# Kernel optimization log

Hardware: AMD Instinct MI355X
Metric: run time of the kernel (lower is better)

## Reference

```python
import jax, jax.numpy as jnp
import numpy as np

NUM_HEADS = 16
NUM_KV_HEADS = 4
HEAD_DIM = 128
HALF_DIM = HEAD_DIM // 2
LAMBDA_INIT = 0.8
LAMBDA_MIN = 0.0
LAMBDA_MAX = 1.0
CAUSAL = True
NORMALIZE_DIFF = True
NEG = -1.0e9


def setup_inputs() -> dict:
    key = jax.random.key(0)
    k1, k2, k3 = jax.random.split(key, 3)
    B, Sq, Sk = 1, 2048, 2048
    query = jax.random.normal(k1, (B, NUM_HEADS, Sq, HEAD_DIM), dtype=jnp.float32)
    key_t = jax.random.normal(k2, (B, NUM_KV_HEADS, Sk, HEAD_DIM), dtype=jnp.float32)
    value = jax.random.normal(k3, (B, NUM_KV_HEADS, Sk, HEAD_DIM), dtype=jnp.float32)
    return {"query": query, "key": key_t, "value": value}


def reference(query, key, value):
    scale = 1.0 / (HALF_DIM ** 0.5)
    lam = jnp.clip(jnp.float32(LAMBDA_INIT), LAMBDA_MIN, LAMBDA_MAX)
    # GQA: repeat KV heads to match query heads
    rep = NUM_HEADS // NUM_KV_HEADS
    k = jnp.repeat(key, rep, axis=1)    # [b,h,k,d]
    v = jnp.repeat(value, rep, axis=1)  # [b,h,k,d]
    q1, q2 = query[..., :HALF_DIM], query[..., HALF_DIM:]
    k1, k2 = k[..., :HALF_DIM], k[..., HALF_DIM:]
    scores1 = jnp.einsum('bhqd,bhkd->bhqk', q1, k1) * scale
    scores2 = jnp.einsum('bhqd,bhkd->bhqk', q2, k2) * scale
    if CAUSAL:
        Sq, Sk = query.shape[2], k.shape[2]
        mask = jnp.tril(jnp.ones((Sq, Sk), dtype=jnp.float32))  # lower-triangular causal
        scores1 = scores1 * mask + (1.0 - mask) * NEG
        scores2 = scores2 * mask + (1.0 - mask) * NEG
    attn1 = jax.nn.softmax(scores1, axis=-1)
    attn2 = jax.nn.softmax(scores2, axis=-1)
    diff_attn = attn1 - lam * attn2
    out = jnp.einsum('bhqk,bhkd->bhqd', diff_attn, v)
    if NORMALIZE_DIFF:
        out = out * (1.0 - LAMBDA_INIT)
    return out
```

## Files before the change

kernel.cpp:

```cpp
#include <hip/hip_runtime.h>

#define NUM_HEADS 16
#define HEAD_DIM  128
#define SEQ       2048

typedef __attribute__((ext_vector_type(8))) unsigned short us8;
typedef __attribute__((ext_vector_type(8))) __bf16 bf16x8;
typedef __attribute__((ext_vector_type(4))) float f32x4;
typedef __attribute__((ext_vector_type(4))) unsigned u32x4;
typedef __attribute__((ext_vector_type(2))) unsigned u32x2;

static __device__ inline unsigned short f2bf(float x) {
    union { float f; unsigned u; } v; v.f = x;
    unsigned r = v.u + 0x7FFFu + ((v.u >> 16) & 1u);
    return (unsigned short)(r >> 16);
}
static __device__ inline float bf2f(unsigned short h) {
    union { float f; unsigned u; } v; v.u = ((unsigned)h) << 16;
    return v.f;
}
static __device__ inline unsigned pk2bf(float a, float b) {
    return (unsigned)f2bf(a) | ((unsigned)f2bf(b) << 16);
}
static __device__ inline float fast_exp2(float x) {
#if __has_builtin(__builtin_amdgcn_exp2f)
    return __builtin_amdgcn_exp2f(x);
#else
    return exp2f(x);
#endif
}
static __device__ inline f32x4 mfma16(us8 a, us8 b, f32x4 c) {
    return __builtin_amdgcn_mfma_f32_16x16x32_bf16(
        __builtin_bit_cast(bf16x8, a), __builtin_bit_cast(bf16x8, b), c, 0, 0, 0);
}

__global__ __launch_bounds__(256)
void prep_kv(const float* __restrict__ K, const float* __restrict__ V,
             unsigned short* __restrict__ Kbf, unsigned short* __restrict__ Vtb)
{
    const int bx = (int)blockIdx.x, t = (int)threadIdx.x;
    __shared__ __align__(16) float Ls[64][130];
    if (bx < 512) {
        const size_t base = ((size_t)bx * 256 + t) * 8;
        float x[8];
        *(float4*)&x[0] = *(const float4*)(K + base);
        *(float4*)&x[4] = *(const float4*)(K + base + 4);
        u32x4 pk;
        #pragma unroll
        for (int j = 0; j < 4; ++j) pk[j] = pk2bf(x[2*j], x[2*j+1]);
        *(us8*)(Kbf + base) = __builtin_bit_cast(us8, pk);
    } else {
        const int b2 = bx - 512, kvh = b2 >> 5, tile = b2 & 31;
        const float* vb = V + ((size_t)kvh * SEQ + tile * 64) * HEAD_DIM;
        #pragma unroll
        for (int i = 0; i < 8; ++i) {
            const int idx = t + i * 256;
            const int r = idx >> 5, c4 = idx & 31;
            *(float4*)&Ls[r][c4 * 4] = *(const float4*)(vb + (size_t)r * HEAD_DIM + c4 * 4);
        }
        __syncthreads();
        const int d = t & 127, kh = t >> 7;
        unsigned pk[16];
        #pragma unroll
        for (int j = 0; j < 16; ++j)
            pk[j] = pk2bf(Ls[kh * 32 + 2*j][d], Ls[kh * 32 + 2*j + 1][d]);
        unsigned short* dst = Vtb + ((size_t)(kvh * 32 + tile) * 128 + d) * 64 + kh * 32;
        #pragma unroll
        for (int blk = 0; blk < 4; ++blk)
            *(us8*)(dst + blk * 8) = *(us8*)&pk[blk * 4];
    }
}

#define KB0 0
#define KB1 16384
#define VB0 32768
#define VB1 49152
#define P_OFF 65536

__global__ __launch_bounds__(256, 2)
void diff_attn_mfma5(const float* __restrict__ Q,
                     const unsigned short* __restrict__ Kbf,
                     const unsigned short* __restrict__ Vtb,
                     float* __restrict__ Out)
{
    __shared__ __align__(16) unsigned char smem[74752];

    const int t    = (int)threadIdx.x;
    const int wv   = t >> 6;
    const int ln   = t & 63;
    const int l15  = ln & 15;
    const int quad = ln >> 4;
    const int mat  = wv >> 1;
    const int rfh  = wv & 1;

    const int bx  = (int)blockIdx.x;
    const int h   = bx & 15;
    const int idx = bx >> 4;
    const int qt  = (idx < 32) ? idx : 95 - idx;
    const int kvh = h >> 2;
    const int q0  = qt * 32;
    const int nkt = (qt >> 1) + 1;

    us8 qhi[2], qlo[2];
    {
        const float* qr = Q + ((size_t)h * SEQ + q0 + rfh * 16 + l15) * HEAD_DIM + mat * 64;
        const float qscale = 0.125f * 1.44269504088896340736f;
        #pragma unroll
        for (int kc = 0; kc < 2; ++kc) {
            const int d0 = kc * 32 + quad * 8;
            float x[8];
            *(float4*)&x[0] = *(const float4*)(qr + d0);
            *(float4*)&x[4] = *(const float4*)(qr + d0 + 4);
            us8 hi8, lo8;
            #pragma unroll
            for (int j = 0; j < 8; ++j) {
                float xs = x[j] * qscale;
                unsigned short hb = f2bf(xs);
                hi8[j] = hb;
                lo8[j] = f2bf(xs - bf2f(hb));
            }
            qhi[kc] = hi8; qlo[kc] = lo8;
        }
    }

    f32x4 o[8];
    #pragma unroll
    for (int i = 0; i < 8; ++i) o[i] = (f32x4)0.f;
    f32x4 rsv = (f32x4)0.f;

    const unsigned short* Kt0 = Kbf + (size_t)kvh * SEQ * HEAD_DIM;
    const unsigned short* Vt0 = Vtb + (size_t)kvh * 32 * 128 * 64;
    unsigned char* Pp = smem + P_OFF + wv * 2304;

    auto issue = [&](int kt, int koff, int voff) {
        #pragma unroll
        for (int i = 0; i < 4; ++i) {
            const int L  = i * 256 + wv * 64 + ln;
            const int r  = L >> 4;
            const int ch = (L & 15) ^ (r & 15);
            const unsigned short* g = Kt0 + (size_t)(kt * 64 + r) * 128 + ch * 8;
            __builtin_amdgcn_global_load_lds(
                (const __attribute__((address_space(1))) unsigned*)g,
                (__attribute__((address_space(3))) unsigned*)(smem + koff + (i * 256 + wv * 64) * 16),
                16, 0, 0);
        }
        #pragma unroll
        for (int i = 0; i < 4; ++i) {
            const int L  = i * 256 + wv * 64 + ln;
            const int r  = L >> 3;
            const int ch = (L & 7) ^ (r & 7);
            const unsigned short* g = Vt0 + (size_t)(kt * 128 + r) * 64 + ch * 8;
            __builtin_amdgcn_global_load_lds(
                (const __attribute__((address_space(1))) unsigned*)g,
                (__attribute__((address_space(3))) unsigned*)(smem + voff + (i * 256 + wv * 64) * 16),
                16, 0, 0);
        }
    };

    issue(0, KB0, VB0);

    for (int kt = 0; kt < nkt; ++kt) {
        const int cur = kt & 1;
        __syncthreads();

        if (kt + 1 < nkt) issue(kt + 1, cur ? KB0 : KB1, cur ? VB0 : VB1);

        const unsigned char* kbase = smem + (cur ? KB1 : KB0);
        const unsigned char* vbase = smem + (cur ? VB1 : VB0);
        const bool lastkt = (kt == nkt - 1);

        #pragma unroll
        for (int c4 = 0; c4 < 4; ++c4) {
            f32x4 s = (f32x4)0.f;
            #pragma unroll
            for (int kc = 0; kc < 2; ++kc) {
                const int r  = c4 * 16 + l15;
                const int ch = (mat * 8 + kc * 4 + quad) ^ l15;
                us8 ak = *(const us8*)(kbase + r * 256 + ch * 16);
                s = mfma16(ak, qhi[kc], s);
                s = mfma16(ak, qlo[kc], s);
            }
            float ev[4];
            if (lastkt) {
                const int kg0 = kt * 64 + c4 * 16 + quad * 4;
                const int qg  = q0 + rfh * 16 + l15;
                #pragma unroll
                for (int rg = 0; rg < 4; ++rg)
                    ev[rg] = ((kg0 + rg) <= qg) ? fast_exp2(s[rg]) : 0.f;
            } else {
                #pragma unroll
                for (int rg = 0; rg < 4; ++rg)
                    ev[rg] = fast_exp2(s[rg]);
            }
            unsigned tr[4];
            #pragma unroll
            for (int rg = 0; rg < 4; ++rg) {
                tr[rg] = __builtin_bit_cast(unsigned, ev[rg]) & 0xffff0000u;
                rsv[rg] += __builtin_bit_cast(float, tr[rg]);
            }
            u32x2 pw;
            pw[0] = (tr[0] >> 16) | tr[1];
            pw[1] = (tr[2] >> 16) | tr[3];
            *(u32x2*)(Pp + l15 * 144 + c4 * 32 + quad * 8) = pw;
        }

        asm volatile("s_waitcnt lgkmcnt(0)" ::: "memory");

        #pragma unroll
        for (int c2 = 0; c2 < 2; ++c2) {
            us8 bp = *(const us8*)(Pp + l15 * 144 + c2 * 64 + quad * 16);
            #pragma unroll
            for (int dt = 0; dt < 8; ++dt) {
                const int r  = dt * 16 + l15;
                const int ch = (c2 * 4 + quad) ^ (r & 7);
                us8 av = *(const us8*)(vbase + r * 128 + ch * 16);
                o[dt] = mfma16(av, bp, o[dt]);
            }
        }
    }

    __syncthreads();

    float rs = (rsv[0] + rsv[1]) + (rsv[2] + rsv[3]);
    rs += __shfl_xor(rs, 16, 64);
    rs += __shfl_xor(rs, 32, 64);
    const float inv = 1.0f / rs;

    float* Cb = (float*)smem;
    if (mat == 1) {
        #pragma unroll
        for (int dt = 0; dt < 8; ++dt) {
            f32x4 v;
            #pragma unroll
            for (int rg = 0; rg < 4; ++rg) v[rg] = o[dt][rg] * inv;
            *(f32x4*)(Cb + (rfh * 16 + l15) * 132 + dt * 16 + quad * 4) = v;
        }
    }
    __syncthreads();
    if (mat == 0) {
        float* ob = Out + ((size_t)h * SEQ + q0 + rfh * 16 + l15) * HEAD_DIM;
        #pragma unroll
        for (int dt = 0; dt < 8; ++dt) {
            const float* cb = Cb + (rfh * 16 + l15) * 132 + dt * 16 + quad * 4;
            float4 r;
            r.x = 0.2f * (o[dt][0] * inv) - 0.16f * cb[0];
            r.y = 0.2f * (o[dt][1] * inv) - 0.16f * cb[1];
            r.z = 0.2f * (o[dt][2] * inv) - 0.16f * cb[2];
            r.w = 0.2f * (o[dt][3] * inv) - 0.16f * cb[3];
            *(float4*)(ob + dt * 16 + quad * 4) = r;
        }
    }
}

extern "C" void kernel_launch(void* const* d_in, const int* in_sizes, int n_in,
                              void* d_out, int out_size, void* d_ws, size_t ws_size,
                              hipStream_t stream) {
    const float* Q = (const float*)d_in[0];
    const float* K = (const float*)d_in[1];
    const float* V = (const float*)d_in[2];
    float* Out = (float*)d_out;

    unsigned short* Kbf = (unsigned short*)d_ws;
    unsigned short* Vtb = Kbf + (size_t)4 * SEQ * HEAD_DIM;

    prep_kv<<<640, 256, 0, stream>>>(K, V, Kbf, Vtb);
    diff_attn_mfma5<<<1024, 256, 0, stream>>>(Q, Kbf, Vtb, Out);
}
```

Before: 124.8 us.

## Switch to 32x32 MFMA, split keys across waves, pair query tiles per block

Replaces the 16x16x32 MFMA path with 32x32x16 bf16 MFMA. Each wave now handles 32 query rows and one 32-key half of the tile, and the P matrix is exchanged through cross-lane shuffles instead of LDS. Each block processes two complementary causal query tiles in sequence, which balances work and halves the grid. A cross-wave reduction of the partial outputs is added in the epilogue, and fully masked diagonal halves are skipped. The cost is more epilogue syncs and LDS traffic, heavier register use for the 16-wide accumulators, and fewer blocks to fill the GPU.

```diff
diff --git a/kernel.cpp b/kernel.cpp
--- a/kernel.cpp
+++ b/kernel.cpp
@@ -7,8 +7,8 @@
 typedef __attribute__((ext_vector_type(8))) unsigned short us8;
 typedef __attribute__((ext_vector_type(8))) __bf16 bf16x8;
 typedef __attribute__((ext_vector_type(4))) float f32x4;
+typedef __attribute__((ext_vector_type(16))) float f32x16;
 typedef __attribute__((ext_vector_type(4))) unsigned u32x4;
-typedef __attribute__((ext_vector_type(2))) unsigned u32x2;
 
 static __device__ inline unsigned short f2bf(float x) {
     union { float f; unsigned u; } v; v.f = x;
@@ -29,8 +29,8 @@
     return exp2f(x);
 #endif
 }
-static __device__ inline f32x4 mfma16(us8 a, us8 b, f32x4 c) {
-    return __builtin_amdgcn_mfma_f32_16x16x32_bf16(
+static __device__ inline f32x16 mfma32(us8 a, us8 b, f32x16 c) {
+    return __builtin_amdgcn_mfma_f32_32x32x16_bf16(
         __builtin_bit_cast(bf16x8, a), __builtin_bit_cast(bf16x8, b), c, 0, 0, 0);
 }
 
@@ -75,39 +75,42 @@
 #define KB1 16384
 #define VB0 32768
 #define VB1 49152
-#define P_OFF 65536
 
 __global__ __launch_bounds__(256, 2)
-void diff_attn_mfma5(const float* __restrict__ Q,
+void diff_attn_mfma6(const float* __restrict__ Q,
                      const unsigned short* __restrict__ Kbf,
                      const unsigned short* __restrict__ Vtb,
                      float* __restrict__ Out)
 {
-    __shared__ __align__(16) unsigned char smem[74752];
-
-    const int t    = (int)threadIdx.x;
-    const int wv   = t >> 6;
-    const int ln   = t & 63;
-    const int l15  = ln & 15;
-    const int quad = ln >> 4;
-    const int mat  = wv >> 1;
-    const int rfh  = wv & 1;
-
-    const int bx  = (int)blockIdx.x;
-    const int h   = bx & 15;
-    const int idx = bx >> 4;
-    const int qt  = (idx < 32) ? idx : 95 - idx;
-    const int kvh = h >> 2;
-    const int q0  = qt * 32;
-    const int nkt = (qt >> 1) + 1;
-
-    us8 qhi[2], qlo[2];
-    {
-        const float* qr = Q + ((size_t)h * SEQ + q0 + rfh * 16 + l15) * HEAD_DIM + mat * 64;
-        const float qscale = 0.125f * 1.44269504088896340736f;
-        #pragma unroll
-        for (int kc = 0; kc < 2; ++kc) {
-            const int d0 = kc * 32 + quad * 8;
+    __shared__ __align__(16) unsigned char smem[65536];
+    __shared__ float rsb[2][2][32];
+
+    const int t   = (int)threadIdx.x;
+    const int wv  = t >> 6;
+    const int ln  = t & 63;
+    const int mat = wv >> 1;
+    const int kh  = wv & 1;
+    const int q   = ln & 31;
+    const int H   = ln >> 5;
+
+    const int bx   = (int)blockIdx.x;
+    const int h    = bx & 15;
+    const int idx  = bx >> 4;
+    const int qtA  = idx, qtB = 63 - idx;
+    const int nktA = (qtA >> 1) + 1;
+    const int kvh  = h >> 2;
+
+    const unsigned short* Kt0 = Kbf + (size_t)kvh * SEQ * HEAD_DIM;
+    const unsigned short* Vt0 = Vtb + (size_t)kvh * 32 * 128 * 64;
+
+    const float qscale = 0.125f * 1.44269504088896340736f;
+
+    us8 qhi[4], qlo[4];
+    auto loadQ = [&](int q0c) {
+        const float* qr = Q + ((size_t)h * SEQ + q0c + q) * HEAD_DIM + mat * 64;
+        #pragma unroll
+        for (int ds = 0; ds < 4; ++ds) {
+            const int d0 = ds * 16 + H * 8;
             float x[8];
             *(float4*)&x[0] = *(const float4*)(qr + d0);
             *(float4*)&x[4] = *(const float4*)(qr + d0 + 4);
@@ -119,137 +122,181 @@
                 hi8[j] = hb;
                 lo8[j] = f2bf(xs - bf2f(hb));
             }
-            qhi[kc] = hi8; qlo[kc] = lo8;
-        }
-    }
-
-    f32x4 o[8];
+            qhi[ds] = hi8; qlo[ds] = lo8;
+        }
+    };
+
+    f32x16 o[4];
+    f32x4 rsv;
     #pragma unroll
-    for (int i = 0; i < 8; ++i) o[i] = (f32x4)0.f;
-    f32x4 rsv = (f32x4)0.f;
-
-    const unsigned short* Kt0 = Kbf + (size_t)kvh * SEQ * HEAD_DIM;
-    const unsigned short* Vt0 = Vtb + (size_t)kvh * 32 * 128 * 64;
-    unsigned char* Pp = smem + P_OFF + wv * 2304;
-
-    auto issue = [&](int kt, int koff, int voff) {
+    for (int i = 0; i < 4; ++i) o[i] = (f32x16)0.f;
+    rsv = (f32x4)0.f;
+
+    auto issue = [&](int kt, int par) {
+        unsigned char* kb = smem + (par ? KB1 : KB0);
+        unsigned char* vb = smem + (par ? VB1 : VB0);
         #pragma unroll
         for (int i = 0; i < 4; ++i) {
-            const int L  = i * 256 + wv * 64 + ln;
-            const int r  = L >> 4;
-            const int ch = (L & 15) ^ (r & 15);
-            const unsigned short* g = Kt0 + (size_t)(kt * 64 + r) * 128 + ch * 8;
+            const int L = i * 256 + t;
+            const int r = L >> 4, g = (L & 15) ^ (r & 15);
+            const unsigned short* gp = Kt0 + (size_t)(kt * 64 + r) * 128 + g * 8;
             __builtin_amdgcn_global_load_lds(
-                (const __attribute__((address_space(1))) unsigned*)g,
-                (__attribute__((address_space(3))) unsigned*)(smem + koff + (i * 256 + wv * 64) * 16),
+                (const __attribute__((address_space(1))) unsigned*)gp,
+                (__attribute__((address_space(3))) unsigned*)(kb + (size_t)(i * 256 + wv * 64) * 16),
                 16, 0, 0);
         }
         #pragma unroll
         for (int i = 0; i < 4; ++i) {
-            const int L  = i * 256 + wv * 64 + ln;
-            const int r  = L >> 3;
-            const int ch = (L & 7) ^ (r & 7);
-            const unsigned short* g = Vt0 + (size_t)(kt * 128 + r) * 64 + ch * 8;
+            const int L = i * 256 + t;
+            const int r = L >> 3, g = (L & 7) ^ (r & 7);
+            const unsigned short* gp = Vt0 + (size_t)(kt * 128 + r) * 64 + g * 8;
             __builtin_amdgcn_global_load_lds(
-                (const __attribute__((address_space(1))) unsigned*)g,
-                (__attribute__((address_space(3))) unsigned*)(smem + voff + (i * 256 + wv * 64) * 16),
+                (const __attribute__((address_space(1))) unsigned*)gp,
+                (__attribute__((address_space(3))) unsigned*)(vb + (size_t)(i * 256 + wv * 64) * 16),
                 16, 0, 0);
         }
     };
 
-    issue(0, KB0, VB0);
-
-    for (int kt = 0; kt < nkt; ++kt) {
-        const int cur = kt & 1;
-        __syncthreads();
-
-        if (kt + 1 < nkt) issue(kt + 1, cur ? KB0 : KB1, cur ? VB0 : VB1);
-
+    auto epilogue = [&](int q0c, int epar) {
+        __syncthreads();
+        float rsc = (rsv[0] + rsv[1]) + (rsv[2] + rsv[3]);
+        rsc += __shfl_xor(rsc, 32, 64);
+        if (ln < 32) rsb[mat][kh][ln] = rsc;
+        float* cbK = (float*)(smem + (epar ? KB1 : KB0));
+        float* cbV = (float*)(smem + (epar ? VB1 : VB0));
+        float* cbM = mat ? cbV : cbK;
+        if (kh == 1) {
+            #pragma unroll
+            for (int db = 0; db < 4; ++db)
+                #pragma unroll
+                for (int i = 0; i < 4; ++i) {
+                    f32x4 v = { o[db][i*4+0], o[db][i*4+1], o[db][i*4+2], o[db][i*4+3] };
+                    *(f32x4*)(cbM + q * 128 + ((((db<<3)+(i<<1)+H) ^ q) << 2)) = v;
+                }
+        }
+        __syncthreads();
+        if (kh == 0) {
+            const float l = rsb[mat][0][q] + rsb[mat][1][q];
+            const float a = mat ? (0.16f / l) : (0.2f / l);
+            #pragma unroll
+            for (int db = 0; db < 4; ++db)
+                #pragma unroll
+                for (int i = 0; i < 4; ++i) {
+                    f32x4 v = *(f32x4*)(cbM + q * 128 + ((((db<<3)+(i<<1)+H) ^ q) << 2));
+                    #pragma unroll
+                    for (int jj = 0; jj < 4; ++jj)
+                        o[db][i*4+jj] = (o[db][i*4+jj] + v[jj]) * a;
+                }
+            if (mat == 1) {
+                #pragma unroll
+                for (int db = 0; db < 4; ++db)
+                    #pragma unroll
+                    for (int i = 0; i < 4; ++i) {
+                        f32x4 v = { o[db][i*4+0], o[db][i*4+1], o[db][i*4+2], o[db][i*4+3] };
+                        *(f32x4*)(cbV + q * 128 + ((((db<<3)+(i<<1)+H) ^ q) << 2)) = v;
+                    }
+            }
+        }
+        __syncthreads();
+        if (wv == 0) {
+            float* ob = Out + ((size_t)h * SEQ + q0c + q) * HEAD_DIM;
+            #pragma unroll
+            for (int db = 0; db < 4; ++db)
+                #pragma unroll
+                for (int i = 0; i < 4; ++i) {
+                    f32x4 v = *(f32x4*)(cbV + q * 128 + ((((db<<3)+(i<<1)+H) ^ q) << 2));
+                    float4 r;
+                    r.x = o[db][i*4+0] - v[0];
+                    r.y = o[db][i*4+1] - v[1];
+                    r.z = o[db][i*4+2] - v[2];
+                    r.w = o[db][i*4+3] - v[3];
+                    *(float4*)(ob + db * 32 + 8 * i + 4 * H) = r;
+                }
+        }
+    };
+
+    int q0 = qtA * 32, qt_cur = qtA;
+    loadQ(q0);
+    issue(0, 0);
+
+    for (int j = 0; j < 33; ++j) {
+        if (j == nktA) {
+            epilogue(q0, (nktA - 1) & 1);
+            q0 = qtB * 32; qt_cur = qtB;
+            loadQ(q0);
+            #pragma unroll
+            for (int i = 0; i < 4; ++i) o[i] = (f32x16)0.f;
+            rsv = (f32x4)0.f;
+        }
+        const int cur = j & 1;
+        __syncthreads();
+        if (j + 1 < 33) issue((j + 1 < nktA) ? j + 1 : j + 1 - nktA, cur ^ 1);
+
+        const int kt = (j < nktA) ? j : j - nktA;
         const unsigned char* kbase = smem + (cur ? KB1 : KB0);
         const unsigned char* vbase = smem + (cur ? VB1 : VB0);
-        const bool lastkt = (kt == nkt - 1);
-
-        #pragma unroll
-        for (int c4 = 0; c4 < 4; ++c4) {
-            f32x4 s = (f32x4)0.f;
-            #pragma unroll
-            for (int kc = 0; kc < 2; ++kc) {
-                const int r  = c4 * 16 + l15;
-                const int ch = (mat * 8 + kc * 4 + quad) ^ l15;
-                us8 ak = *(const us8*)(kbase + r * 256 + ch * 16);
-                s = mfma16(ak, qhi[kc], s);
-                s = mfma16(ak, qlo[kc], s);
-            }
-            float ev[4];
-            if (lastkt) {
-                const int kg0 = kt * 64 + c4 * 16 + quad * 4;
-                const int qg  = q0 + rfh * 16 + l15;
-                #pragma unroll
-                for (int rg = 0; rg < 4; ++rg)
-                    ev[rg] = ((kg0 + rg) <= qg) ? fast_exp2(s[rg]) : 0.f;
+        const bool diag  = (j == nktA - 1) || (j == 32);
+        const int  qpar  = qt_cur & 1;
+        const bool skipw = diag && (qpar == 0) && (kh == 1);
+        const bool triw  = diag && (kh == qpar);
+
+        if (!skipw) {
+            f32x16 s = (f32x16)0.f;
+            const int krow = kh * 32 + q;
+            #pragma unroll
+            for (int ds = 0; ds < 4; ++ds) {
+                us8 ak = *(const us8*)(kbase +
+                          ((krow << 4) + ((mat * 8 + ds * 2 + H) ^ (krow & 15))) * 16);
+                s = mfma32(ak, qhi[ds], s);
+                s = mfma32(ak, qlo[ds], s);
+            }
+            unsigned c[16];
+            if (triw) {
+                const int kg0 = kt * 64 + kh * 32 + 4 * H;
+                const int qg  = q0 + q;
+                #pragma unroll
+                for (int r = 0; r < 16; ++r) {
+                    const int kg = kg0 + (r & 3) + ((r >> 2) << 3);
+                    float e = (kg <= qg) ? fast_exp2(s[r]) : 0.f;
+                    c[r] = __builtin_bit_cast(unsigned, e) & 0xffff0000u;
+                    rsv[r & 3] += __builtin_bit_cast(float, c[r]);
+                }
             } else {
                 #pragma unroll
-                for (int rg = 0; rg < 4; ++rg)
-                    ev[rg] = fast_exp2(s[rg]);
-            }
-            unsigned tr[4];
-            #pragma unroll
-            for (int rg = 0; rg < 4; ++rg) {
-                tr[rg] = __builtin_bit_cast(unsigned, ev[rg]) & 0xffff0000u;
-                rsv[rg] += __builtin_bit_cast(float, tr[rg]);
-            }
-            u32x2 pw;
-            pw[0] = (tr[0] >> 16) | tr[1];
-            pw[1] = (tr[2] >> 16) | tr[3];
-            *(u32x2*)(Pp + l15 * 144 + c4 * 32 + quad * 8) = pw;
-        }
-
-        asm volatile("s_waitcnt lgkmcnt(0)" ::: "memory");
-
-        #pragma unroll
-        for (int c2 = 0; c2 < 2; ++c2) {
-            us8 bp = *(const us8*)(Pp + l15 * 144 + c2 * 64 + quad * 16);
-            #pragma unroll
-            for (int dt = 0; dt < 8; ++dt) {
-                const int r  = dt * 16 + l15;
-                const int ch = (c2 * 4 + quad) ^ (r & 7);
-                us8 av = *(const us8*)(vbase + r * 128 + ch * 16);
-                o[dt] = mfma16(av, bp, o[dt]);
+                for (int r = 0; r < 16; ++r) {
+                    float e = fast_exp2(s[r]);
+                    c[r] = __builtin_bit_cast(unsigned, e) & 0xffff0000u;
+                    rsv[r & 3] += __builtin_bit_cast(float, c[r]);
+                }
+            }
+            #pragma unroll
+            for (int ks = 0; ks < 2; ++ks) {
+                const unsigned pA = (c[8*ks+0] >> 16) | c[8*ks+1];
+                const unsigned pB = (c[8*ks+2] >> 16) | c[8*ks+3];
+                const unsigned pC = (c[8*ks+4] >> 16) | c[8*ks+5];
+                const unsigned pD = (c[8*ks+6] >> 16) | c[8*ks+7];
+                const unsigned x1 = H ? pA : pC;
+                const unsigned x2 = H ? pB : pD;
+                const unsigned t1 = (unsigned)__shfl_xor((int)x1, 32, 64);
+                const unsigned t2 = (unsigned)__shfl_xor((int)x2, 32, 64);
+                u32x4 bw;
+                bw[0] = H ? t1 : pA;
+                bw[1] = H ? t2 : pB;
+                bw[2] = H ? pC : t1;
+                bw[3] = H ? pD : t2;
+                const us8 bp = __builtin_bit_cast(us8, bw);
+                const int gb = kh * 4 + ks * 2 + H;
+                #pragma unroll
+                for (int db = 0; db < 4; ++db) {
+                    const int r = db * 32 + q;
+                    us8 av = *(const us8*)(vbase + ((r << 3) + (gb ^ (r & 7))) * 16);
+                    o[db] = mfma32(av, bp, o[db]);
+                }
             }
         }
     }
 
-    __syncthreads();
-
-    float rs = (rsv[0] + rsv[1]) + (rsv[2] + rsv[3]);
-    rs += __shfl_xor(rs, 16, 64);
-    rs += __shfl_xor(rs, 32, 64);
-    const float inv = 1.0f / rs;
-
-    float* Cb = (float*)smem;
-    if (mat == 1) {
-        #pragma unroll
-        for (int dt = 0; dt < 8; ++dt) {
-            f32x4 v;
-            #pragma unroll
-            for (int rg = 0; rg < 4; ++rg) v[rg] = o[dt][rg] * inv;
-            *(f32x4*)(Cb + (rfh * 16 + l15) * 132 + dt * 16 + quad * 4) = v;
-        }
-    }
-    __syncthreads();
-    if (mat == 0) {
-        float* ob = Out + ((size_t)h * SEQ + q0 + rfh * 16 + l15) * HEAD_DIM;
-        #pragma unroll
-        for (int dt = 0; dt < 8; ++dt) {
-            const float* cb = Cb + (rfh * 16 + l15) * 132 + dt * 16 + quad * 4;
-            float4 r;
-            r.x = 0.2f * (o[dt][0] * inv) - 0.16f * cb[0];
-            r.y = 0.2f * (o[dt][1] * inv) - 0.16f * cb[1];
-            r.z = 0.2f * (o[dt][2] * inv) - 0.16f * cb[2];
-            r.w = 0.2f * (o[dt][3] * inv) - 0.16f * cb[3];
-            *(float4*)(ob + dt * 16 + quad * 4) = r;
-        }
-    }
+    epilogue(q0, 0);
 }
 
 extern "C" void kernel_launch(void* const* d_in, const int* in_sizes, int n_in,
@@ -264,5 +311,5 @@
     unsigned short* Vtb = Kbf + (size_t)4 * SEQ * HEAD_DIM;
 
     prep_kv<<<640, 256, 0, stream>>>(K, V, Kbf, Vtb);
-    diff_attn_mfma5<<<1024, 256, 0, stream>>>(Q, Kbf, Vtb, Out);
-}
+    diff_attn_mfma6<<<512, 256, 0, stream>>>(Q, Kbf, Vtb, Out);
+}
```

Result: no change. 125.3 us (+0.4%).
